# Performance work log

Hardware: AMD Instinct MI355X
Metric: run time of the kernel (lower is better)

Reference implementation:

```python
import jax, jax.numpy as jnp
import numpy as np

N, E, D = 50000, 800000, 128  # nodes, edges, in_dim == out_dim


def setup_inputs() -> dict:
    key = jax.random.key(0)
    ks = jax.random.split(key, 10)
    s = 1.0 / np.sqrt(2 * D)
    t = 1.0 / np.sqrt(D)
    return {
        "x": jax.random.normal(ks[0], (N, D), dtype=jnp.float32),
        "edge_index": jax.random.randint(ks[1], (2, E), 0, N, dtype=jnp.int64),
        # message_net: Linear(2D -> D), ReLU, Linear(D -> D)
        "mW1": jax.random.uniform(ks[2], (2 * D, D), jnp.float32, -s, s),
        "mb1": jax.random.uniform(ks[3], (D,), jnp.float32, -s, s),
        "mW2": jax.random.uniform(ks[4], (D, D), jnp.float32, -t, t),
        "mb2": jax.random.uniform(ks[5], (D,), jnp.float32, -t, t),
        # update_net: Linear(D + D -> D), ReLU, Linear(D -> D)
        "uW1": jax.random.uniform(ks[6], (2 * D, D), jnp.float32, -s, s),
        "ub1": jax.random.uniform(ks[7], (D,), jnp.float32, -s, s),
        "uW2": jax.random.uniform(ks[8], (D, D), jnp.float32, -t, t),
        "ub2": jax.random.uniform(ks[9], (D,), jnp.float32, -t, t),
    }


def reference(x, edge_index, mW1, mb1, mW2, mb2, uW1, ub1, uW2, ub2):
    row, col = edge_index[0], edge_index[1]
    # gather endpoints -> [E, 2D]
    msg_in = jnp.concatenate([x[row], x[col]], axis=-1)
    h = jax.nn.relu(msg_in @ mW1 + mb1)
    messages = h @ mW2 + mb2  # [E, D]
    # scatter-add messages to destination nodes (index_add_ on col)
    aggregated = jax.ops.segment_sum(messages, col, num_segments=x.shape[0])
    upd_in = jnp.concatenate([x, aggregated], axis=-1)  # [N, 2D]
    g = jax.nn.relu(upd_in @ uW1 + ub1)
    return jax.nn.relu(g @ uW2 + ub2)
```

## Files before the change

kernel.cpp:

```cpp
#include <hip/hip_runtime.h>
#include <stdint.h>

typedef unsigned short ushort_t;

#define NNODES 50000
#define NEDGES 800000
#define DD 128
#define EB 128

typedef short bf16x8 __attribute__((ext_vector_type(8)));
typedef float f32x16 __attribute__((ext_vector_type(16)));

#define XH_OFF    0u
#define XL_OFF    12800000u
#define W1P_OFF   25600000u
#define W2P_OFF   25731072u
#define WS_MIN    25796608u
#define DEG_OFF   25796608u
#define ELIST_OFF 25996800u
#define CUR_OFF   29196800u
#define WS_CSR    29396992u

#define PQ_OFF2   0u
#define W1P_OFF2  51200000u
#define U2P_OFF2  51331072u
#define WNP_OFF2  51396608u
#define W2U_OFF2  51527680u
#define VV_OFF2   51593216u
#define DEG_OFF2  51593728u
#define CUR_OFF2  51793920u
#define BSUM_OFF2 51994112u
#define EL_OFF2   51994368u
#define WS_NEW    55194368u
#define WS_NEW2   58394368u

#define NB_SCAN 49

__global__ void zero_kernel(float4* __restrict__ p, int n4) {
    int i = blockIdx.x * blockDim.x + threadIdx.x;
    if (i < n4) p[i] = make_float4(0.f, 0.f, 0.f, 0.f);
}
__global__ void zero_i32(int* __restrict__ p, int n) {
    int i = blockIdx.x * blockDim.x + threadIdx.x;
    if (i < n) p[i] = 0;
}

__device__ inline void bf16_split(float f, ushort_t& hi, ushort_t& lo) {
    uint32_t b = __float_as_uint(f);
    uint32_t hb = b & 0xFFFF0000u;
    hi = (ushort_t)(b >> 16);
    float lof = f - __uint_as_float(hb);
    lo = (ushort_t)(__float_as_uint(lof) >> 16);
}

__global__ void pack_x(const float* __restrict__ x,
                       ushort_t* __restrict__ xh, ushort_t* __restrict__ xl) {
    int i = blockIdx.x * blockDim.x + threadIdx.x;
    if (i >= NNODES * DD) return;
    ushort_t h, l;
    bf16_split(x[i], h, l);
    xh[i] = h; xl[i] = l;
}

__global__ void pack_w(const float* __restrict__ W, ushort_t* __restrict__ wp,
                       int K) {
    int i = blockIdx.x * blockDim.x + threadIdx.x;
    if (i >= K * 128) return;
    int k = i >> 7, n = i & 127;
    int base = (k >> 4) * 4096 + ((((k >> 3) & 1) * 128 + n) << 3) + (k & 7);
    ushort_t h, l;
    bf16_split(W[i], h, l);
    wp[base] = h; wp[base + 2048] = l;
}

__global__ void pack3(const float* __restrict__ mW1, const float* __restrict__ uW2,
                      const float* __restrict__ uW1,
                      ushort_t* __restrict__ w1p, ushort_t* __restrict__ u2p,
                      ushort_t* __restrict__ wnp) {
    int i = blockIdx.x * blockDim.x + threadIdx.x;
    const float* W; ushort_t* wp; int li;
    if (i < 32768)      { W = mW1; wp = w1p; li = i; }
    else if (i < 49152) { W = uW2; wp = u2p; li = i - 32768; }
    else                { W = uW1; wp = wnp; li = i - 49152; }
    int k = li >> 7, n = li & 127;
    int base = (k >> 4) * 4096 + ((((k >> 3) & 1) * 128 + n) << 3) + (k & 7);
    ushort_t h, l;
    bf16_split(W[li], h, l);
    wp[base] = h; wp[base + 2048] = l;
}

__global__ void hist_kernel(const int* __restrict__ ei, int* __restrict__ deg) {
    int i = blockIdx.x * blockDim.x + threadIdx.x;
    if (i < NEDGES) atomicAdd(&deg[ei[NEDGES + i]], 1);
}

__global__ __launch_bounds__(1024)
void scan_kernel(const int* __restrict__ deg, int* __restrict__ cursor) {
    __shared__ int part[1024];
    const int t = threadIdx.x;
    const int CH = 49;
    int s = 0;
#pragma unroll 1
    for (int i = 0; i < CH; ++i) {
        int idx = t * CH + i;
        if (idx < NNODES) s += deg[idx];
    }
    part[t] = s;
    __syncthreads();
    for (int d = 1; d < 1024; d <<= 1) {
        int v = (t >= d) ? part[t - d] : 0;
        __syncthreads();
        part[t] += v;
        __syncthreads();
    }
    int run = (t == 0) ? 0 : part[t - 1];
#pragma unroll 1
    for (int i = 0; i < CH; ++i) {
        int idx = t * CH + i;
        if (idx < NNODES) {
            cursor[idx] = run;
            run += deg[idx];
        }
    }
}

__global__ __launch_bounds__(1024)
void scanA(const int* __restrict__ deg, int* __restrict__ cur,
           int* __restrict__ bsum) {
    __shared__ int sm[1024];
    const int t = threadIdx.x;
    const int idx = blockIdx.x * 1024 + t;
    int d = (idx < NNODES) ? deg[idx] : 0;
    sm[t] = d;
    __syncthreads();
    for (int off = 1; off < 1024; off <<= 1) {
        int v = 0;
        if (t >= off) v = sm[t - off];
        __syncthreads();
        sm[t] += v;
        __syncthreads();
    }
    if (idx < NNODES) cur[idx] = sm[t];
    if (t == 1023) bsum[blockIdx.x] = sm[1023];
}
__global__ void scanB(int* __restrict__ bsum, int nb) {
    if (threadIdx.x == 0) {
        int run = 0;
        for (int i = 0; i < nb; ++i) { int v = bsum[i]; bsum[i] = run; run += v; }
    }
}
__global__ __launch_bounds__(1024)
void scanC(const int* __restrict__ deg, int* __restrict__ cur,
           const int* __restrict__ bsum) {
    const int idx = blockIdx.x * 1024 + threadIdx.x;
    if (idx < NNODES) cur[idx] = cur[idx] - deg[idx] + bsum[blockIdx.x];
}
__global__ __launch_bounds__(1024)
void scanC2(const int* __restrict__ deg, int* __restrict__ cur,
            const int* __restrict__ bsum) {
    int pre = 0;
#pragma unroll 1
    for (int j = 0; j < blockIdx.x; ++j) pre += bsum[j];
    const int idx = blockIdx.x * 1024 + threadIdx.x;
    if (idx < NNODES) cur[idx] = cur[idx] - deg[idx] + pre;
}

__global__ void fill_kernel(const int* __restrict__ ei, int* __restrict__ cursor,
                            int* __restrict__ elist) {
    int i = blockIdx.x * blockDim.x + threadIdx.x;
    if (i < NEDGES) {
        int pos = atomicAdd(&cursor[ei[NEDGES + i]], 1);
        elist[pos] = i;
    }
}
__global__ void fill2_kernel(const int* __restrict__ ei, int* __restrict__ cursor,
                             int2* __restrict__ ep) {
    int i = blockIdx.x * blockDim.x + threadIdx.x;
    if (i < NEDGES) {
        int c = ei[NEDGES + i];
        int pos = atomicAdd(&cursor[c], 1);
        ep[pos] = make_int2(ei[i], c);
    }
}

__global__ void w2u_kernel(const float* __restrict__ W2,
                           const float* __restrict__ U1, float* __restrict__ W2U) {
    int id = blockIdx.x * 256 + threadIdx.x;
    if (id >= 128 * 128) return;
    int i = id >> 7, j = id & 127;
    float s = 0.f;
    for (int k = 0; k < 128; ++k) s += W2[i * 128 + k] * U1[(128 + k) * 128 + j];
    W2U[id] = s;
}
__global__ void vvec_kernel(const float* __restrict__ b2,
                            const float* __restrict__ U1, float* __restrict__ vv) {
    int j = threadIdx.x;
    if (j >= 128) return;
    float s = 0.f;
    for (int k = 0; k < 128; ++k) s += b2[k] * U1[(128 + k) * 128 + j];
    vv[j] = s;
}
__global__ void w2u_vv(const float* __restrict__ W2, const float* __restrict__ b2,
                       const float* __restrict__ U1,
                       float* __restrict__ W2U, float* __restrict__ vv) {
    if (blockIdx.x < 64) {
        int id = blockIdx.x * 256 + threadIdx.x;
        int i = id >> 7, j = id & 127;
        float s = 0.f;
        for (int k = 0; k < 128; ++k)
            s += W2[i * 128 + k] * U1[(128 + k) * 128 + j];
        W2U[id] = s;
    } else if (threadIdx.x < 128) {
        int j = threadIdx.x;
        float s = 0.f;
        for (int k = 0; k < 128; ++k)
            s += b2[k] * U1[(128 + k) * 128 + j];
        vv[j] = s;
    }
}

__global__ __launch_bounds__(256)
void pq_gemm(const float* __restrict__ x, const ushort_t* __restrict__ w1p,
             const float* __restrict__ b1, float* __restrict__ PQ) {
    __shared__ __align__(16) ushort_t Wst[4096];
    const int t = threadIdx.x, w = t >> 6, l = t & 63;
    const int lh = l >> 5, ln = l & 31;
    const int base = blockIdx.x * 128;
    const int c = blockIdx.y;
    const int row = base + w * 32 + ln;
    const float* ax = x + (size_t)min(row, NNODES - 1) * DD;
    const ushort_t* wt = w1p + c * 8 * 4096;

    f32x16 acc[4];
#pragma unroll
    for (int tt = 0; tt < 4; ++tt)
#pragma unroll
        for (int q = 0; q < 16; ++q) acc[tt][q] = 0.f;

    float4 pfh = *(const float4*)(wt + t * 8);
    float4 pfl = *(const float4*)(wt + 2048 + t * 8);
    for (int u = 0; u < 8; ++u) {
        __syncthreads();
        *(float4*)(Wst + t * 8)        = pfh;
        *(float4*)(Wst + 2048 + t * 8) = pfl;
        float4 a0 = *(const float4*)(ax + u * 16 + lh * 8);
        float4 a1 = *(const float4*)(ax + u * 16 + lh * 8 + 4);
        if (u < 7) {
            pfh = *(const float4*)(wt + (u + 1) * 4096 + t * 8);
            pfl = *(const float4*)(wt + (u + 1) * 4096 + 2048 + t * 8);
        }
        float av[8] = {a0.x, a0.y, a0.z, a0.w, a1.x, a1.y, a1.z, a1.w};
        bf16x8 a_hi, a_lo;
#pragma unroll
        for (int q = 0; q < 8; ++q) {
            ushort_t h, lo16;
            bf16_split(av[q], h, lo16);
            a_hi[q] = (short)h; a_lo[q] = (short)lo16;
        }
        __syncthreads();
#pragma unroll
        for (int tt = 0; tt < 4; ++tt) {
            const int boff = (lh * 128 + tt * 32 + ln) * 8;
            bf16x8 bh = *(const bf16x8*)(Wst + boff);
            bf16x8 bl = *(const bf16x8*)(Wst + 2048 + boff);
            acc[tt] = __builtin_amdgcn_mfma_f32_32x32x16_bf16(a_hi, bh, acc[tt], 0, 0, 0);
            acc[tt] = __builtin_amdgcn_mfma_f32_32x32x16_bf16(a_hi, bl, acc[tt], 0, 0, 0);
            acc[tt] = __builtin_amdgcn_mfma_f32_32x32x16_bf16(a_lo, bh, acc[tt], 0, 0, 0);
        }
    }
    float bias[4];
#pragma unroll
    for (int tt = 0; tt < 4; ++tt)
        bias[tt] = (c == 0) ? b1[tt * 32 + ln] : 0.f;
#pragma unroll
    for (int tt = 0; tt < 4; ++tt) {
#pragma unroll
        for (int r = 0; r < 16; ++r) {
            int mrow = w * 32 + (r & 3) + 8 * (r >> 2) + 4 * lh;
            int n = base + mrow;
            if (n < NNODES)
                PQ[(size_t)n * 256 + c * 128 + tt * 32 + ln] = acc[tt][r] + bias[tt];
        }
    }
}

#define EW_C 4
__global__ __launch_bounds__(256)
void edge_ew(const float* __restrict__ PQ, const int* __restrict__ ei,
             const int* __restrict__ elist, float* Hsum) {
    const int t = threadIdx.x, w = t >> 6, l = t & 63;
    const int start = blockIdx.x * 512 + w * 128;
    if (start >= NEDGES) return;
    const int end = min(start + 128, NEDGES);

    float sx = 0.f, sy = 0.f;
    int cur = -1;
    int rv[EW_C] = {0, 0, 0, 0}, cv[EW_C] = {0, 0, 0, 0};
    float px[EW_C] = {0, 0, 0, 0}, py[EW_C] = {0, 0, 0, 0};
    float qx[EW_C] = {0, 0, 0, 0}, qy[EW_C] = {0, 0, 0, 0};

    const int navail = min(EW_C, end - start);
#pragma unroll
    for (int i = 0; i < EW_C; ++i)
        if (i < navail) {
            int e = elist[start + i];
            rv[i] = ei[e]; cv[i] = ei[NEDGES + e];
        }
#pragma unroll
    for (int i = 0; i < EW_C; ++i)
        if (i < navail) {
            float2 p = *(const float2*)(PQ + (size_t)rv[i] * 256 + 2 * l);
            float2 q = *(const float2*)(PQ + (size_t)cv[i] * 256 + 128 + 2 * l);
            px[i] = p.x; py[i] = p.y; qx[i] = q.x; qy[i] = q.y;
        }

    for (int pos = start; pos < end; pos += EW_C) {
        const int cnt = min(EW_C, end - pos);
        int nn = end - (pos + EW_C);
        nn = nn < 0 ? 0 : (nn > EW_C ? EW_C : nn);
        int nrv[EW_C] = {0, 0, 0, 0}, ncv[EW_C] = {0, 0, 0, 0};
        float npx[EW_C] = {0, 0, 0, 0}, npy[EW_C] = {0, 0, 0, 0};
        float nqx[EW_C] = {0, 0, 0, 0}, nqy[EW_C] = {0, 0, 0, 0};
#pragma unroll
        for (int i = 0; i < EW_C; ++i)
            if (i < nn) {
                int e = elist[pos + EW_C + i];
                nrv[i] = ei[e]; ncv[i] = ei[NEDGES + e];
            }
#pragma unroll
        for (int i = 0; i < EW_C; ++i)
            if (i < nn) {
                float2 p = *(const float2*)(PQ + (size_t)nrv[i] * 256 + 2 * l);
                float2 q = *(const float2*)(PQ + (size_t)ncv[i] * 256 + 128 + 2 * l);
                npx[i] = p.x; npy[i] = p.y; nqx[i] = q.x; nqy[i] = q.y;
            }
#pragma unroll
        for (int i = 0; i < EW_C; ++i)
            if (i < cnt) {
                if (cv[i] != cur) {
                    if (cur >= 0) {
                        atomicAdd(Hsum + (size_t)cur * DD + 2 * l,     sx);
                        atomicAdd(Hsum + (size_t)cur * DD + 2 * l + 1, sy);
                    }
                    sx = 0.f; sy = 0.f; cur = cv[i];
                }
                sx += fmaxf(px[i] + qx[i], 0.f);
                sy += fmaxf(py[i] + qy[i], 0.f);
            }
#pragma unroll
        for (int i = 0; i < EW_C; ++i) {
            rv[i] = nrv[i]; cv[i] = ncv[i];
            px[i] = npx[i]; py[i] = npy[i]; qx[i] = nqx[i]; qy[i] = nqy[i];
        }
    }
    if (cur >= 0) {
        atomicAdd(Hsum + (size_t)cur * DD + 2 * l,     sx);
        atomicAdd(Hsum + (size_t)cur * DD + 2 * l + 1, sy);
    }
}

__global__ __launch_bounds__(256)
void edge_pn(const float* __restrict__ PQ, const int2* __restrict__ ep,
             const int* __restrict__ endp, const int* __restrict__ deg,
             float* __restrict__ Hsum) {
    const int n = blockIdx.x * 4 + (threadIdx.x >> 6);
    if (n >= NNODES) return;
    const int l = threadIdx.x & 63;
    const int end = endp[n];
    const int start = end - deg[n];

    const float2 q = *(const float2*)(PQ + (size_t)n * 256 + 128 + 2 * l);
    float sx = 0.f, sy = 0.f;

    int s0[4];
    float2 p0[4];
    const int c0 = min(4, end - start);
#pragma unroll
    for (int i = 0; i < 4; ++i) s0[i] = (i < c0) ? ep[start + i].x : 0;
#pragma unroll
    for (int i = 0; i < 4; ++i)
        if (i < c0) p0[i] = *(const float2*)(PQ + (size_t)s0[i] * 256 + 2 * l);

    for (int e = start; e < end; e += 4) {
        const int cnt = min(4, end - e);
        int nn = end - (e + 4);
        nn = nn < 0 ? 0 : (nn > 4 ? 4 : nn);
        int s1[4];
        float2 p1[4];
#pragma unroll
        for (int i = 0; i < 4; ++i) s1[i] = (i < nn) ? ep[e + 4 + i].x : 0;
#pragma unroll
        for (int i = 0; i < 4; ++i)
            if (i < nn) p1[i] = *(const float2*)(PQ + (size_t)s1[i] * 256 + 2 * l);
#pragma unroll
        for (int i = 0; i < 4; ++i)
            if (i < cnt) {
                sx += fmaxf(p0[i].x + q.x, 0.f);
                sy += fmaxf(p0[i].y + q.y, 0.f);
            }
#pragma unroll
        for (int i = 0; i < 4; ++i) { s0[i] = s1[i]; p0[i] = p1[i]; }
    }

    Hsum[(size_t)n * DD + 2 * l]     = sx;
    Hsum[(size_t)n * DD + 2 * l + 1] = sy;
}

__device__ inline int hs_idx(int m, int j) {
    return m * 128 + ((((j >> 2) ^ (m & 31)) << 2) | (j & 3));
}

__global__ __launch_bounds__(256, 2)
void node_mfma(const float* __restrict__ x, float* outHsum,
               const ushort_t* __restrict__ wnp, const ushort_t* __restrict__ u2p,
               const int* __restrict__ deg, const float* __restrict__ vv,
               const float* __restrict__ ub1, const float* __restrict__ ub2) {
    __shared__ __align__(16) float    Hs[128 * 128];
    __shared__ __align__(16) ushort_t Wst[4096];
    const int t = threadIdx.x, w = t >> 6, l = t & 63;
    const int lh = l >> 5, ln = l & 31;
    const int base = blockIdx.x * 128;
    const int row = base + w * 32 + ln;
    const int rowc = min(row, NNODES - 1);
    const float* ax = x + (size_t)rowc * DD;
    const float* ah = outHsum + (size_t)rowc * DD;

    f32x16 acc[4];
#pragma unroll
    for (int tt = 0; tt < 4; ++tt)
#pragma unroll
        for (int q = 0; q < 16; ++q) acc[tt][q] = 0.f;

    float4 pfh = *(const float4*)(wnp + t * 8);
    float4 pfl = *(const float4*)(wnp + 2048 + t * 8);
    for (int u = 0; u < 16; ++u) {
        __syncthreads();
        *(float4*)(Wst + t * 8)        = pfh;
        *(float4*)(Wst + 2048 + t * 8) = pfl;
        const int k = u * 16 + lh * 8;
        const float* src = (k < 128) ? (ax + k) : (ah + (k - 128));
        float4 a0 = *(const float4*)(src);
        float4 a1 = *(const float4*)(src + 4);
        if (u < 15) {
            pfh = *(const float4*)(wnp + (u + 1) * 4096 + t * 8);
            pfl = *(const float4*)(wnp + (u + 1) * 4096 + 2048 + t * 8);
        }
        float av[8] = {a0.x, a0.y, a0.z, a0.w, a1.x, a1.y, a1.z, a1.w};
        bf16x8 a_hi, a_lo;
#pragma unroll
        for (int q = 0; q < 8; ++q) {
            ushort_t h, lo16;
            bf16_split(av[q], h, lo16);
            a_hi[q] = (short)h; a_lo[q] = (short)lo16;
        }
        __syncthreads();
#pragma unroll
        for (int tt = 0; tt < 4; ++tt) {
            const int boff = (lh * 128 + tt * 32 + ln) * 8;
            bf16x8 bh = *(const bf16x8*)(Wst + boff);
            bf16x8 bl = *(const bf16x8*)(Wst + 2048 + boff);
            acc[tt] = __builtin_amdgcn_mfma_f32_32x32x16_bf16(a_hi, bh, acc[tt], 0, 0, 0);
            acc[tt] = __builtin_amdgcn_mfma_f32_32x32x16_bf16(a_hi, bl, acc[tt], 0, 0, 0);
            acc[tt] = __builtin_amdgcn_mfma_f32_32x32x16_bf16(a_lo, bh, acc[tt], 0, 0, 0);
        }
    }

    float4 pfh2 = *(const float4*)(u2p + t * 8);
    float4 pfl2 = *(const float4*)(u2p + 2048 + t * 8);

    float b1v[4], vvv[4];
#pragma unroll
    for (int tt = 0; tt < 4; ++tt) {
        b1v[tt] = ub1[tt * 32 + ln];
        vvv[tt] = vv[tt * 32 + ln];
    }
#pragma unroll
    for (int tt = 0; tt < 4; ++tt) {
#pragma unroll
        for (int r = 0; r < 16; ++r) {
            int mrow = w * 32 + (r & 3) + 8 * (r >> 2) + 4 * lh;
            int n = min(base + mrow, NNODES - 1);
            float dg = (float)deg[n];
            float g = acc[tt][r] + b1v[tt] + dg * vvv[tt];
            Hs[hs_idx(mrow, tt * 32 + ln)] = fmaxf(g, 0.f);
            acc[tt][r] = 0.f;
        }
    }

    for (int u = 0; u < 8; ++u) {
        __syncthreads();
        *(float4*)(Wst + t * 8)        = pfh2;
        *(float4*)(Wst + 2048 + t * 8) = pfl2;
        if (u < 7) {
            pfh2 = *(const float4*)(u2p + (u + 1) * 4096 + t * 8);
            pfl2 = *(const float4*)(u2p + (u + 1) * 4096 + 2048 + t * 8);
        }
        __syncthreads();
        const int m  = w * 32 + ln;
        const int s0 = u * 4 + lh * 2;
        float4 f0 = *(const float4*)(Hs + m * 128 + (((s0    ) ^ ln) << 2));
        float4 f1 = *(const float4*)(Hs + m * 128 + (((s0 + 1) ^ ln) << 2));
        float fv[8] = {f0.x, f0.y, f0.z, f0.w, f1.x, f1.y, f1.z, f1.w};
        bf16x8 a_hi, a_lo;
#pragma unroll
        for (int q = 0; q < 8; ++q) {
            ushort_t h, lo16;
            bf16_split(fv[q], h, lo16);
            a_hi[q] = (short)h; a_lo[q] = (short)lo16;
        }
#pragma unroll
        for (int tt = 0; tt < 4; ++tt) {
            const int boff = (lh * 128 + tt * 32 + ln) * 8;
            bf16x8 bh = *(const bf16x8*)(Wst + boff);
            bf16x8 bl = *(const bf16x8*)(Wst + 2048 + boff);
            acc[tt] = __builtin_amdgcn_mfma_f32_32x32x16_bf16(a_hi, bh, acc[tt], 0, 0, 0);
            acc[tt] = __builtin_amdgcn_mfma_f32_32x32x16_bf16(a_hi, bl, acc[tt], 0, 0, 0);
            acc[tt] = __builtin_amdgcn_mfma_f32_32x32x16_bf16(a_lo, bh, acc[tt], 0, 0, 0);
        }
    }

    float b2v[4];
#pragma unroll
    for (int tt = 0; tt < 4; ++tt) b2v[tt] = ub2[tt * 32 + ln];
#pragma unroll
    for (int tt = 0; tt < 4; ++tt) {
#pragma unroll
        for (int r = 0; r < 16; ++r) {
            int mrow = w * 32 + (r & 3) + 8 * (r >> 2) + 4 * lh;
            int n = base + mrow;
            if (n < NNODES)
                outHsum[(size_t)n * DD + tt * 32 + ln] =
                    fmaxf(acc[tt][r] + b2v[tt], 0.f);
        }
    }
}

template <int MODE>
__global__ __launch_bounds__(256, 2)
void edge_mfma(const ushort_t* __restrict__ xh, const ushort_t* __restrict__ xl,
               const ushort_t* __restrict__ w1p, const ushort_t* __restrict__ w2p,
               const int* __restrict__ ei, const int* __restrict__ elist,
               const float* __restrict__ b1, const float* __restrict__ b2,
               float* agg) {
    __shared__ __align__(16) float    Hsl[128 * 128];
    __shared__ __align__(16) ushort_t Wst[4096];
    const int t  = threadIdx.x;
    const int w  = t >> 6;
    const int l  = t & 63;
    const int lh = l >> 5;
    const int ln = l & 31;
    int eg;
    if (MODE == 1) eg = elist[blockIdx.x * EB + w * 32 + ln];
    else           eg = blockIdx.x * EB + w * 32 + ln;
    const int rv = ei[eg];
    const int cv = ei[NEDGES + eg];
    float bias1[4], bias2[4];
#pragma unroll
    for (int tt = 0; tt < 4; ++tt) {
        bias1[tt] = b1[tt * 32 + ln];
        bias2[tt] = b2[tt * 32 + ln];
    }
    f32x16 acc[4];
#pragma unroll
    for (int tt = 0; tt < 4; ++tt)
#pragma unroll
        for (int q = 0; q < 16; ++q) acc[tt][q] = 0.f;
    bf16x8 a_hi_next = *(const bf16x8*)(xh + (size_t)rv * DD + lh * 8);
    bf16x8 a_lo_next = *(const bf16x8*)(xl + (size_t)rv * DD + lh * 8);
    float4 pfh = *(const float4*)(w1p + t * 8);
    float4 pfl = *(const float4*)(w1p + 2048 + t * 8);
    for (int u = 0; u < 16; ++u) {
        __syncthreads();
        *(float4*)(Wst + t * 8)        = pfh;
        *(float4*)(Wst + 2048 + t * 8) = pfl;
        bf16x8 a_hi = a_hi_next, a_lo = a_lo_next;
        if (u < 15) {
            pfh = *(const float4*)(w1p + (u + 1) * 4096 + t * 8);
            pfl = *(const float4*)(w1p + (u + 1) * 4096 + 2048 + t * 8);
            int kk = (u + 1) * 16 + lh * 8;
            const int node = (kk < 128) ? rv : cv;
            const int off  = kk & 127;
            a_hi_next = *(const bf16x8*)(xh + (size_t)node * DD + off);
            a_lo_next = *(const bf16x8*)(xl + (size_t)node * DD + off);
        }
        __syncthreads();
#pragma unroll
        for (int tt = 0; tt < 4; ++tt) {
            const int boff = (lh * 128 + tt * 32 + ln) * 8;
            bf16x8 bh = *(const bf16x8*)(Wst + boff);
            bf16x8 bl = *(const bf16x8*)(Wst + 2048 + boff);
            acc[tt] = __builtin_amdgcn_mfma_f32_32x32x16_bf16(a_hi, bh, acc[tt], 0, 0, 0);
            acc[tt] = __builtin_amdgcn_mfma_f32_32x32x16_bf16(a_hi, bl, acc[tt], 0, 0, 0);
            acc[tt] = __builtin_amdgcn_mfma_f32_32x32x16_bf16(a_lo, bh, acc[tt], 0, 0, 0);
        }
    }
    pfh = *(const float4*)(w2p + t * 8);
    pfl = *(const float4*)(w2p + 2048 + t * 8);
#pragma unroll
    for (int tt = 0; tt < 4; ++tt) {
#pragma unroll
        for (int r = 0; r < 16; ++r) {
            int mrow = w * 32 + (r & 3) + 8 * (r >> 2) + 4 * lh;
            int j    = tt * 32 + ln;
            Hsl[hs_idx(mrow, j)] = fmaxf(acc[tt][r] + bias1[tt], 0.f);
            acc[tt][r] = 0.f;
        }
    }
    for (int u = 0; u < 8; ++u) {
        __syncthreads();
        *(float4*)(Wst + t * 8)        = pfh;
        *(float4*)(Wst + 2048 + t * 8) = pfl;
        if (u < 7) {
            pfh = *(const float4*)(w2p + (u + 1) * 4096 + t * 8);
            pfl = *(const float4*)(w2p + (u + 1) * 4096 + 2048 + t * 8);
        }
        __syncthreads();
        const int m  = w * 32 + ln;
        const int s0 = u * 4 + lh * 2;
        float4 f0 = *(const float4*)(Hsl + m * 128 + (((s0    ) ^ ln) << 2));
        float4 f1 = *(const float4*)(Hsl + m * 128 + (((s0 + 1) ^ ln) << 2));
        float fv[8] = {f0.x, f0.y, f0.z, f0.w, f1.x, f1.y, f1.z, f1.w};
        bf16x8 a_hi, a_lo;
#pragma unroll
        for (int q = 0; q < 8; ++q) {
            ushort_t h, lo16;
            bf16_split(fv[q], h, lo16);
            a_hi[q] = (short)h;
            a_lo[q] = (short)lo16;
        }
#pragma unroll
        for (int tt = 0; tt < 4; ++tt) {
            const int boff = (lh * 128 + tt * 32 + ln) * 8;
            bf16x8 bh = *(const bf16x8*)(Wst + boff);
            bf16x8 bl = *(const bf16x8*)(Wst + 2048 + boff);
            acc[tt] = __builtin_amdgcn_mfma_f32_32x32x16_bf16(a_hi, bh, acc[tt], 0, 0, 0);
            acc[tt] = __builtin_amdgcn_mfma_f32_32x32x16_bf16(a_hi, bl, acc[tt], 0, 0, 0);
            acc[tt] = __builtin_amdgcn_mfma_f32_32x32x16_bf16(a_lo, bh, acc[tt], 0, 0, 0);
        }
    }
    if (MODE == 1) {
        float s[4] = {0.f, 0.f, 0.f, 0.f};
        int cur = __shfl(cv, 0, 64);
#pragma unroll
        for (int row = 0; row < 32; ++row) {
            const int r = (row & 3) | ((row >> 3) << 2);
            const int h = (row >> 2) & 1;
            int nd = __shfl(cv, row, 64);
            if (nd != cur) {
                if (lh == 0) {
#pragma unroll
                    for (int tt = 0; tt < 4; ++tt)
                        atomicAdd(agg + (size_t)cur * DD + tt * 32 + ln, s[tt]);
                }
#pragma unroll
                for (int tt = 0; tt < 4; ++tt) s[tt] = 0.f;
                cur = nd;
            }
#pragma unroll
            for (int tt = 0; tt < 4; ++tt) {
                float mine  = acc[tt][r];
                float other = __shfl_xor(mine, 32, 64);
                float v = (h == lh) ? mine : other;
                s[tt] += v + bias2[tt];
            }
        }
        if (lh == 0) {
#pragma unroll
            for (int tt = 0; tt < 4; ++tt)
                atomicAdd(agg + (size_t)cur * DD + tt * 32 + ln, s[tt]);
        }
    } else {
        int cn[16];
#pragma unroll
        for (int r = 0; r < 16; ++r) {
            int mr = (r & 3) + 8 * (r >> 2) + 4 * lh;
            cn[r] = __shfl(cv, mr, 64);
        }
#pragma unroll
        for (int tt = 0; tt < 4; ++tt) {
#pragma unroll
            for (int r = 0; r < 16; ++r) {
                atomicAdd(agg + (size_t)cn[r] * DD + tt * 32 + ln,
                          acc[tt][r] + bias2[tt]);
            }
        }
    }
}

#define TE 64
#define KT 16
#define AX_S 260
#define HS_S 132
#define AX_WORDS (TE * AX_S)
#define WT_WORDS (KT * DD)
#define SMEM_WORDS (AX_WORDS + WT_WORDS + TE)

__global__ __launch_bounds__(256, 2)
void node_kernel(const float* __restrict__ x,
                 float* aggout,
                 const float* __restrict__ U1, const float* __restrict__ c1,
                 const float* __restrict__ U2, const float* __restrict__ c2) {
    __shared__ float smem[SMEM_WORDS];
    float* Ax = smem;
    float* Hss = smem;
    float* Wt = smem + AX_WORDS;
    const int t = threadIdx.x;
    const int base = blockIdx.x * TE;
    {
        const int e = t & 63;
        const int q = t >> 6;
        const int n = base + e;
        const bool valid = n < NNODES;
        const float* s1 = x + (size_t)n * DD;
        const float* s2 = aggout + (size_t)n * DD;
#pragma unroll
        for (int ci = 0; ci < 16; ++ci) {
            const int k4 = ci * 4 + q;
            float4 v = make_float4(0.f, 0.f, 0.f, 0.f);
            if (valid) {
                if (k4 < 32) v = *(const float4*)(s1 + k4 * 4);
                else         v = *(const float4*)(s2 + (k4 - 32) * 4);
            }
            *(float4*)(Ax + e * AX_S + k4 * 4) = v;
        }
    }
    const int jg = t & 31;
    const int eg2 = t >> 5;
    const int j0 = jg * 4;
    const float4 b1v = *(const float4*)(c1 + j0);
    const float4 b2v = *(const float4*)(c2 + j0);
    float acc[8][4];
#pragma unroll
    for (int i = 0; i < 8; ++i)
        acc[i][0] = acc[i][1] = acc[i][2] = acc[i][3] = 0.f;
    for (int kb = 0; kb < 256 / KT; ++kb) {
        __syncthreads();
        {
            const float* src = U1 + kb * KT * DD;
#pragma unroll
            for (int u = 0; u < 2; ++u) {
                const int f4i = u * 256 + t;
                *(float4*)(Wt + f4i * 4) = *(const float4*)(src + f4i * 4);
            }
        }
        __syncthreads();
        float4 Bc[KT];
#pragma unroll
        for (int kk = 0; kk < KT; ++kk)
            Bc[kk] = *(const float4*)(Wt + kk * DD + j0);
#pragma unroll
        for (int i = 0; i < 8; ++i) {
            const float* arow = Ax + (i * 8 + eg2) * AX_S + kb * KT;
            float a[KT];
#pragma unroll
            for (int kc = 0; kc < KT / 4; ++kc) {
                const float4 av = *(const float4*)(arow + kc * 4);
                a[kc * 4 + 0] = av.x; a[kc * 4 + 1] = av.y;
                a[kc * 4 + 2] = av.z; a[kc * 4 + 3] = av.w;
            }
#pragma unroll
            for (int kk = 0; kk < KT; ++kk) {
                acc[i][0] = fmaf(a[kk], Bc[kk].x, acc[i][0]);
                acc[i][1] = fmaf(a[kk], Bc[kk].y, acc[i][1]);
                acc[i][2] = fmaf(a[kk], Bc[kk].z, acc[i][2]);
                acc[i][3] = fmaf(a[kk], Bc[kk].w, acc[i][3]);
            }
        }
    }
    __syncthreads();
#pragma unroll
    for (int i = 0; i < 8; ++i) {
        float4 h;
        h.x = fmaxf(acc[i][0] + b1v.x, 0.f);
        h.y = fmaxf(acc[i][1] + b1v.y, 0.f);
        h.z = fmaxf(acc[i][2] + b1v.z, 0.f);
        h.w = fmaxf(acc[i][3] + b1v.w, 0.f);
        *(float4*)(Hss + (i * 8 + eg2) * HS_S + j0) = h;
        acc[i][0] = acc[i][1] = acc[i][2] = acc[i][3] = 0.f;
    }
    for (int kb = 0; kb < DD / KT; ++kb) {
        __syncthreads();
        {
            const float* src = U2 + kb * KT * DD;
#pragma unroll
            for (int u = 0; u < 2; ++u) {
                const int f4i = u * 256 + t;
                *(float4*)(Wt + f4i * 4) = *(const float4*)(src + f4i * 4);
            }
        }
        __syncthreads();
        float4 Bc[KT];
#pragma unroll
        for (int kk = 0; kk < KT; ++kk)
            Bc[kk] = *(const float4*)(Wt + kk * DD + j0);
#pragma unroll
        for (int i = 0; i < 8; ++i) {
            const float* arow = Hss + (i * 8 + eg2) * HS_S + kb * KT;
            float a[KT];
#pragma unroll
            for (int kc = 0; kc < KT / 4; ++kc) {
                const float4 av = *(const float4*)(arow + kc * 4);
                a[kc * 4 + 0] = av.x; a[kc * 4 + 1] = av.y;
                a[kc * 4 + 2] = av.z; a[kc * 4 + 3] = av.w;
            }
#pragma unroll
            for (int kk = 0; kk < KT; ++kk) {
                acc[i][0] = fmaf(a[kk], Bc[kk].x, acc[i][0]);
                acc[i][1] = fmaf(a[kk], Bc[kk].y, acc[i][1]);
                acc[i][2] = fmaf(a[kk], Bc[kk].z, acc[i][2]);
                acc[i][3] = fmaf(a[kk], Bc[kk].w, acc[i][3]);
            }
        }
    }
#pragma unroll
    for (int i = 0; i < 8; ++i) {
        const int n = base + i * 8 + eg2;
        if (n < NNODES) {
            float4 o;
            o.x = fmaxf(acc[i][0] + b2v.x, 0.f);
            o.y = fmaxf(acc[i][1] + b2v.y, 0.f);
            o.z = fmaxf(acc[i][2] + b2v.z, 0.f);
            o.w = fmaxf(acc[i][3] + b2v.w, 0.f);
            *(float4*)(aggout + (size_t)n * DD + j0) = o;
        }
    }
}

extern "C" void kernel_launch(void* const* d_in, const int* in_sizes, int n_in,
                              void* d_out, int out_size, void* d_ws, size_t ws_size,
                              hipStream_t stream) {
    const float* x   = (const float*)d_in[0];
    const int*   ei  = (const int*)d_in[1];
    const float* mW1 = (const float*)d_in[2];
    const float* mb1 = (const float*)d_in[3];
    const float* mW2 = (const float*)d_in[4];
    const float* mb2 = (const float*)d_in[5];
    const float* uW1 = (const float*)d_in[6];
    const float* ub1 = (const float*)d_in[7];
    const float* uW2 = (const float*)d_in[8];
    const float* ub2 = (const float*)d_in[9];
    float* out = (float*)d_out;

    const int n4 = NNODES * DD / 4;

    if (ws_size >= (size_t)WS_NEW) {
        float*    PQ   = (float*)((char*)d_ws + PQ_OFF2);
        ushort_t* w1p  = (ushort_t*)((char*)d_ws + W1P_OFF2);
        ushort_t* u2p  = (ushort_t*)((char*)d_ws + U2P_OFF2);
        ushort_t* wnp  = (ushort_t*)((char*)d_ws + WNP_OFF2);
        float*    W2U  = (float*)((char*)d_ws + W2U_OFF2);
        float*    vv   = (float*)((char*)d_ws + VV_OFF2);
        int*      deg  = (int*)((char*)d_ws + DEG_OFF2);
        int*      curb = (int*)((char*)d_ws + CUR_OFF2);
        int*      bsum = (int*)((char*)d_ws + BSUM_OFF2);

        if (ws_size >= (size_t)WS_NEW2) {
            int2* ep = (int2*)((char*)d_ws + EL_OFF2);
            zero_i32<<<(50048 + 255) / 256, 256, 0, stream>>>(deg, 50048);
            hist_kernel<<<(NEDGES + 255) / 256, 256, 0, stream>>>(ei, deg);
            scanA<<<NB_SCAN, 1024, 0, stream>>>(deg, curb, bsum);
            scanC2<<<NB_SCAN, 1024, 0, stream>>>(deg, curb, bsum);
            fill2_kernel<<<(NEDGES + 255) / 256, 256, 0, stream>>>(ei, curb, ep);
            pack3<<<256, 256, 0, stream>>>(mW1, uW2, uW1, w1p, u2p, wnp);
            w2u_vv<<<65, 256, 0, stream>>>(mW2, mb2, uW1, W2U, vv);
            pack_w<<<(128 * 128 + 255) / 256, 256, 0, stream>>>(W2U, wnp + 32768, 128);
            pq_gemm<<<dim3(391, 2), 256, 0, stream>>>(x, w1p, mb1, PQ);
            edge_pn<<<(NNODES + 3) / 4, 256, 0, stream>>>(PQ, ep, curb, deg, out);
            node_mfma<<<391, 256, 0, stream>>>(x, out, wnp, u2p, deg, vv, ub1, ub2);
        } else {
            int* elst = (int*)((char*)d_ws + EL_OFF2);
            zero_kernel<<<(n4 + 255) / 256, 256, 0, stream>>>((float4*)out, n4);
            zero_i32<<<(50048 + 255) / 256, 256, 0, stream>>>(deg, 50048);
            hist_kernel<<<(NEDGES + 255) / 256, 256, 0, stream>>>(ei, deg);
            scanA<<<NB_SCAN, 1024, 0, stream>>>(deg, curb, bsum);
            scanB<<<1, 64, 0, stream>>>(bsum, NB_SCAN);
            scanC<<<NB_SCAN, 1024, 0, stream>>>(deg, curb, bsum);
            fill_kernel<<<(NEDGES + 255) / 256, 256, 0, stream>>>(ei, curb, elst);
            pack_w<<<(256 * 128 + 255) / 256, 256, 0, stream>>>(mW1, w1p, 256);
            pack_w<<<(128 * 128 + 255) / 256, 256, 0, stream>>>(uW2, u2p, 128);
            w2u_kernel<<<64, 256, 0, stream>>>(mW2, uW1, W2U);
            vvec_kernel<<<1, 128, 0, stream>>>(mb2, uW1, vv);
            pack_w<<<(128 * 128 + 255) / 256, 256, 0, stream>>>(uW1, wnp, 128);
            pack_w<<<(128 * 128 + 255) / 256, 256, 0, stream>>>(W2U, wnp + 32768, 128);
            pq_gemm<<<dim3(391, 2), 256, 0, stream>>>(x, w1p, mb1, PQ);
            edge_ew<<<(NEDGES + 511) / 512, 256, 0, stream>>>(PQ, ei, elst, out);
            node_mfma<<<391, 256, 0, stream>>>(x, out, wnp, u2p, deg, vv, ub1, ub2);
        }
        return;
    }

    zero_kernel<<<(n4 + 255) / 256, 256, 0, stream>>>((float4*)out, n4);
    if (ws_size >= (size_t)WS_MIN) {
        ushort_t* xh  = (ushort_t*)((char*)d_ws + XH_OFF);
        ushort_t* xl  = (ushort_t*)((char*)d_ws + XL_OFF);
        ushort_t* w1p = (ushort_t*)((char*)d_ws + W1P_OFF);
        ushort_t* w2p = (ushort_t*)((char*)d_ws + W2P_OFF);
        pack_x<<<(NNODES * DD + 255) / 256, 256, 0, stream>>>(x, xh, xl);
        pack_w<<<(256 * 128 + 255) / 256, 256, 0, stream>>>(mW1, w1p, 256);
        pack_w<<<(128 * 128 + 255) / 256, 256, 0, stream>>>(mW2, w2p, 128);
        if (ws_size >= (size_t)WS_CSR) {
            int* deg    = (int*)((char*)d_ws + DEG_OFF);
            int* elist  = (int*)((char*)d_ws + ELIST_OFF);
            int* cursor = (int*)((char*)d_ws + CUR_OFF);
            zero_i32<<<(50048 + 255) / 256, 256, 0, stream>>>(deg, 50048);
            hist_kernel<<<(NEDGES + 255) / 256, 256, 0, stream>>>(ei, deg);
            scan_kernel<<<1, 1024, 0, stream>>>(deg, cursor);
            fill_kernel<<<(NEDGES + 255) / 256, 256, 0, stream>>>(ei, cursor, elist);
            edge_mfma<1><<<NEDGES / EB, 256, 0, stream>>>(
                xh, xl, w1p, w2p, ei, elist, mb1, mb2, out);
        } else {
            edge_mfma<0><<<NEDGES / EB, 256, 0, stream>>>(
                xh, xl, w1p, w2p, ei, (const int*)nullptr, mb1, mb2, out);
        }
    }
    node_kernel<<<(NNODES + TE - 1) / TE, 256, 0, stream>>>(x, out, uW1, ub1,
                                                            uW2, ub2);
}
```

Before: 322.0 us.

## Merge prep kernels, shrink CSR edge list, retile node MLP to 64-row blocks

```diff
diff --git a/kernel.cpp b/kernel.cpp
--- a/kernel.cpp
+++ b/kernel.cpp
@@ -73,20 +73,25 @@
     wp[base] = h; wp[base + 2048] = l;
 }
 
-__global__ void pack3(const float* __restrict__ mW1, const float* __restrict__ uW2,
+__global__ void prep0(const float* __restrict__ mW1, const float* __restrict__ uW2,
                       const float* __restrict__ uW1,
                       ushort_t* __restrict__ w1p, ushort_t* __restrict__ u2p,
-                      ushort_t* __restrict__ wnp) {
-    int i = blockIdx.x * blockDim.x + threadIdx.x;
-    const float* W; ushort_t* wp; int li;
-    if (i < 32768)      { W = mW1; wp = w1p; li = i; }
-    else if (i < 49152) { W = uW2; wp = u2p; li = i - 32768; }
-    else                { W = uW1; wp = wnp; li = i - 49152; }
-    int k = li >> 7, n = li & 127;
-    int base = (k >> 4) * 4096 + ((((k >> 3) & 1) * 128 + n) << 3) + (k & 7);
-    ushort_t h, l;
-    bf16_split(W[li], h, l);
-    wp[base] = h; wp[base + 2048] = l;
+                      ushort_t* __restrict__ wnp, int* __restrict__ deg) {
+    if (blockIdx.x < 256) {
+        int i = blockIdx.x * 256 + threadIdx.x;
+        const float* W; ushort_t* wp; int li;
+        if (i < 32768)      { W = mW1; wp = w1p; li = i; }
+        else if (i < 49152) { W = uW2; wp = u2p; li = i - 32768; }
+        else                { W = uW1; wp = wnp; li = i - 49152; }
+        int k = li >> 7, n = li & 127;
+        int base = (k >> 4) * 4096 + ((((k >> 3) & 1) * 128 + n) << 3) + (k & 7);
+        ushort_t h, l;
+        bf16_split(W[li], h, l);
+        wp[base] = h; wp[base + 2048] = l;
+    } else {
+        int j = (blockIdx.x - 256) * 256 + threadIdx.x;
+        if (j < 50048) deg[j] = 0;
+    }
 }
 
 __global__ void hist_kernel(const int* __restrict__ ei, int* __restrict__ deg) {
@@ -173,13 +178,12 @@
         elist[pos] = i;
     }
 }
-__global__ void fill2_kernel(const int* __restrict__ ei, int* __restrict__ cursor,
-                             int2* __restrict__ ep) {
+__global__ void fill3_kernel(const int* __restrict__ ei, int* __restrict__ cursor,
+                             int* __restrict__ srcs) {
     int i = blockIdx.x * blockDim.x + threadIdx.x;
     if (i < NEDGES) {
-        int c = ei[NEDGES + i];
-        int pos = atomicAdd(&cursor[c], 1);
-        ep[pos] = make_int2(ei[i], c);
+        int pos = atomicAdd(&cursor[ei[NEDGES + i]], 1);
+        srcs[pos] = ei[i];
     }
 }
 
@@ -200,16 +204,19 @@
     for (int k = 0; k < 128; ++k) s += b2[k] * U1[(128 + k) * 128 + j];
     vv[j] = s;
 }
-__global__ void w2u_vv(const float* __restrict__ W2, const float* __restrict__ b2,
-                       const float* __restrict__ U1,
-                       float* __restrict__ W2U, float* __restrict__ vv) {
+__global__ void w2u_vv_pack(const float* __restrict__ W2, const float* __restrict__ b2,
+                            const float* __restrict__ U1,
+                            ushort_t* __restrict__ wnp2, float* __restrict__ vv) {
     if (blockIdx.x < 64) {
         int id = blockIdx.x * 256 + threadIdx.x;
         int i = id >> 7, j = id & 127;
         float s = 0.f;
         for (int k = 0; k < 128; ++k)
             s += W2[i * 128 + k] * U1[(128 + k) * 128 + j];
-        W2U[id] = s;
+        int base = (i >> 4) * 4096 + ((((i >> 3) & 1) * 128 + j) << 3) + (i & 7);
+        ushort_t h, l;
+        bf16_split(s, h, l);
+        wnp2[base] = h; wnp2[base + 2048] = l;
     } else if (threadIdx.x < 128) {
         int j = threadIdx.x;
         float s = 0.f;
@@ -360,9 +367,9 @@
 }
 
 __global__ __launch_bounds__(256)
-void edge_pn(const float* __restrict__ PQ, const int2* __restrict__ ep,
-             const int* __restrict__ endp, const int* __restrict__ deg,
-             float* __restrict__ Hsum) {
+void edge_pn2(const float* __restrict__ PQ, const int* __restrict__ srcs,
+              const int* __restrict__ endp, const int* __restrict__ deg,
+              float* __restrict__ Hsum) {
     const int n = blockIdx.x * 4 + (threadIdx.x >> 6);
     if (n >= NNODES) return;
     const int l = threadIdx.x & 63;
@@ -376,7 +383,7 @@
     float2 p0[4];
     const int c0 = min(4, end - start);
 #pragma unroll
-    for (int i = 0; i < 4; ++i) s0[i] = (i < c0) ? ep[start + i].x : 0;
+    for (int i = 0; i < 4; ++i) s0[i] = (i < c0) ? srcs[start + i] : 0;
 #pragma unroll
     for (int i = 0; i < 4; ++i)
         if (i < c0) p0[i] = *(const float2*)(PQ + (size_t)s0[i] * 256 + 2 * l);
@@ -388,7 +395,7 @@
         int s1[4];
         float2 p1[4];
 #pragma unroll
-        for (int i = 0; i < 4; ++i) s1[i] = (i < nn) ? ep[e + 4 + i].x : 0;
+        for (int i = 0; i < 4; ++i) s1[i] = (i < nn) ? srcs[e + 4 + i] : 0;
 #pragma unroll
         for (int i = 0; i < 4; ++i)
             if (i < nn) p1[i] = *(const float2*)(PQ + (size_t)s1[i] * 256 + 2 * l);
@@ -408,6 +415,145 @@
 
 __device__ inline int hs_idx(int m, int j) {
     return m * 128 + ((((j >> 2) ^ (m & 31)) << 2) | (j & 3));
+}
+
+__global__ __launch_bounds__(128)
+void node_mfma2(const float* __restrict__ x, float* outHsum,
+                const ushort_t* __restrict__ wnp, const ushort_t* __restrict__ u2p,
+                const int* __restrict__ deg, const float* __restrict__ vv,
+                const float* __restrict__ ub1, const float* __restrict__ ub2) {
+    __shared__ __align__(16) float    Hs[64 * 128];
+    __shared__ __align__(16) ushort_t Wst[4096];
+    const int t = threadIdx.x, w = t >> 6, l = t & 63;
+    const int lh = l >> 5, ln = l & 31;
+    const int base = blockIdx.x * 64;
+    const int row = base + w * 32 + ln;
+    const int rowc = min(row, NNODES - 1);
+    const float* ax = x + (size_t)rowc * DD;
+    const float* ah = outHsum + (size_t)rowc * DD;
+
+    f32x16 acc[4];
+#pragma unroll
+    for (int tt = 0; tt < 4; ++tt)
+#pragma unroll
+        for (int q = 0; q < 16; ++q) acc[tt][q] = 0.f;
+
+    float4 pfh0 = *(const float4*)(wnp + t * 8);
+    float4 pfh1 = *(const float4*)(wnp + (t + 128) * 8);
+    float4 pfl0 = *(const float4*)(wnp + 2048 + t * 8);
+    float4 pfl1 = *(const float4*)(wnp + 2048 + (t + 128) * 8);
+    for (int u = 0; u < 16; ++u) {
+        __syncthreads();
+        *(float4*)(Wst + t * 8)                = pfh0;
+        *(float4*)(Wst + (t + 128) * 8)        = pfh1;
+        *(float4*)(Wst + 2048 + t * 8)         = pfl0;
+        *(float4*)(Wst + 2048 + (t + 128) * 8) = pfl1;
+        const int k = u * 16 + lh * 8;
+        const float* src = (k < 128) ? (ax + k) : (ah + (k - 128));
+        float4 a0 = *(const float4*)(src);
+        float4 a1 = *(const float4*)(src + 4);
+        if (u < 15) {
+            const ushort_t* nx = wnp + (u + 1) * 4096;
+            pfh0 = *(const float4*)(nx + t * 8);
+            pfh1 = *(const float4*)(nx + (t + 128) * 8);
+            pfl0 = *(const float4*)(nx + 2048 + t * 8);
+            pfl1 = *(const float4*)(nx + 2048 + (t + 128) * 8);
+        }
+        float av[8] = {a0.x, a0.y, a0.z, a0.w, a1.x, a1.y, a1.z, a1.w};
+        bf16x8 a_hi, a_lo;
+#pragma unroll
+        for (int q = 0; q < 8; ++q) {
+            ushort_t h, lo16;
+            bf16_split(av[q], h, lo16);
+            a_hi[q] = (short)h; a_lo[q] = (short)lo16;
+        }
+        __syncthreads();
+#pragma unroll
+        for (int tt = 0; tt < 4; ++tt) {
+            const int boff = (lh * 128 + tt * 32 + ln) * 8;
+            bf16x8 bh = *(const bf16x8*)(Wst + boff);
+            bf16x8 bl = *(const bf16x8*)(Wst + 2048 + boff);
+            acc[tt] = __builtin_amdgcn_mfma_f32_32x32x16_bf16(a_hi, bh, acc[tt], 0, 0, 0);
+            acc[tt] = __builtin_amdgcn_mfma_f32_32x32x16_bf16(a_hi, bl, acc[tt], 0, 0, 0);
+            acc[tt] = __builtin_amdgcn_mfma_f32_32x32x16_bf16(a_lo, bh, acc[tt], 0, 0, 0);
+        }
+    }
+
+    float4 p2h0 = *(const float4*)(u2p + t * 8);
+    float4 p2h1 = *(const float4*)(u2p + (t + 128) * 8);
+    float4 p2l0 = *(const float4*)(u2p + 2048 + t * 8);
+    float4 p2l1 = *(const float4*)(u2p + 2048 + (t + 128) * 8);
+
+    float b1v[4], vvv[4];
+#pragma unroll
+    for (int tt = 0; tt < 4; ++tt) {
+        b1v[tt] = ub1[tt * 32 + ln];
+        vvv[tt] = vv[tt * 32 + ln];
+    }
+#pragma unroll
+    for (int tt = 0; tt < 4; ++tt) {
+#pragma unroll
+        for (int r = 0; r < 16; ++r) {
+            int mrow = w * 32 + (r & 3) + 8 * (r >> 2) + 4 * lh;
+            int n = min(base + mrow, NNODES - 1);
+            float dg = (float)deg[n];
+            float g = acc[tt][r] + b1v[tt] + dg * vvv[tt];
+            Hs[hs_idx(mrow, tt * 32 + ln)] = fmaxf(g, 0.f);
+            acc[tt][r] = 0.f;
+        }
+    }
+
+    for (int u = 0; u < 8; ++u) {
+        __syncthreads();
+        *(float4*)(Wst + t * 8)                = p2h0;
+        *(float4*)(Wst + (t + 128) * 8)        = p2h1;
+        *(float4*)(Wst + 2048 + t * 8)         = p2l0;
+        *(float4*)(Wst + 2048 + (t + 128) * 8) = p2l1;
+        if (u < 7) {
+            const ushort_t* nx = u2p + (u + 1) * 4096;
+            p2h0 = *(const float4*)(nx + t * 8);
+            p2h1 = *(const float4*)(nx + (t + 128) * 8);
+            p2l0 = *(const float4*)(nx + 2048 + t * 8);
+            p2l1 = *(const float4*)(nx + 2048 + (t + 128) * 8);
+        }
+        __syncthreads();
+        const int m  = w * 32 + ln;
+        const int s0 = u * 4 + lh * 2;
+        float4 f0 = *(const float4*)(Hs + m * 128 + (((s0    ) ^ ln) << 2));
+        float4 f1 = *(const float4*)(Hs + m * 128 + (((s0 + 1) ^ ln) << 2));
+        float fv[8] = {f0.x, f0.y, f0.z, f0.w, f1.x, f1.y, f1.z, f1.w};
+        bf16x8 a_hi, a_lo;
+#pragma unroll
+        for (int q = 0; q < 8; ++q) {
+            ushort_t h, lo16;
+            bf16_split(fv[q], h, lo16);
+            a_hi[q] = (short)h; a_lo[q] = (short)lo16;
+        }
+#pragma unroll
+        for (int tt = 0; tt < 4; ++tt) {
+            const int boff = (lh * 128 + tt * 32 + ln) * 8;
+            bf16x8 bh = *(const bf16x8*)(Wst + boff);
+            bf16x8 bl = *(const bf16x8*)(Wst + 2048 + boff);
+            acc[tt] = __builtin_amdgcn_mfma_f32_32x32x16_bf16(a_hi, bh, acc[tt], 0, 0, 0);
+            acc[tt] = __builtin_amdgcn_mfma_f32_32x32x16_bf16(a_hi, bl, acc[tt], 0, 0, 0);
+            acc[tt] = __builtin_amdgcn_mfma_f32_32x32x16_bf16(a_lo, bh, acc[tt], 0, 0, 0);
+        }
+    }
+
+    float b2v[4];
+#pragma unroll
+    for (int tt = 0; tt < 4; ++tt) b2v[tt] = ub2[tt * 32 + ln];
+#pragma unroll
+    for (int tt = 0; tt < 4; ++tt) {
+#pragma unroll
+        for (int r = 0; r < 16; ++r) {
+            int mrow = w * 32 + (r & 3) + 8 * (r >> 2) + 4 * lh;
+            int n = base + mrow;
+            if (n < NNODES)
+                outHsum[(size_t)n * DD + tt * 32 + ln] =
+                    fmaxf(acc[tt][r] + b2v[tt], 0.f);
+        }
+    }
 }
 
 __global__ __launch_bounds__(256, 2)
@@ -415,7 +561,7 @@
                const ushort_t* __restrict__ wnp, const ushort_t* __restrict__ u2p,
                const int* __restrict__ deg, const float* __restrict__ vv,
                const float* __restrict__ ub1, const float* __restrict__ ub2) {
-    __shared__ __align__(16) float    Hs[128 * 128];
+    __shared__ __align__(16) float    Hs2[128 * 128];
     __shared__ __align__(16) ushort_t Wst[4096];
     const int t = threadIdx.x, w = t >> 6, l = t & 63;
     const int lh = l >> 5, ln = l & 31;
@@ -482,7 +628,7 @@
             int n = min(base + mrow, NNODES - 1);
             float dg = (float)deg[n];
             float g = acc[tt][r] + b1v[tt] + dg * vvv[tt];
-            Hs[hs_idx(mrow, tt * 32 + ln)] = fmaxf(g, 0.f);
+            Hs2[hs_idx(mrow, tt * 32 + ln)] = fmaxf(g, 0.f);
             acc[tt][r] = 0.f;
         }
     }
@@ -498,8 +644,8 @@
         __syncthreads();
         const int m  = w * 32 + ln;
         const int s0 = u * 4 + lh * 2;
-        float4 f0 = *(const float4*)(Hs + m * 128 + (((s0    ) ^ ln) << 2));
-        float4 f1 = *(const float4*)(Hs + m * 128 + (((s0 + 1) ^ ln) << 2));
+        float4 f0 = *(const float4*)(Hs2 + m * 128 + (((s0    ) ^ ln) << 2));
+        float4 f1 = *(const float4*)(Hs2 + m * 128 + (((s0 + 1) ^ ln) << 2));
         float fv[8] = {f0.x, f0.y, f0.z, f0.w, f1.x, f1.y, f1.z, f1.w};
         bf16x8 a_hi, a_lo;
 #pragma unroll
@@ -855,18 +1001,17 @@
         int*      bsum = (int*)((char*)d_ws + BSUM_OFF2);
 
         if (ws_size >= (size_t)WS_NEW2) {
-            int2* ep = (int2*)((char*)d_ws + EL_OFF2);
-            zero_i32<<<(50048 + 255) / 256, 256, 0, stream>>>(deg, 50048);
+            int* srcs = (int*)((char*)d_ws + EL_OFF2);
+            prep0<<<452, 256, 0, stream>>>(mW1, uW2, uW1, w1p, u2p, wnp, deg);
             hist_kernel<<<(NEDGES + 255) / 256, 256, 0, stream>>>(ei, deg);
             scanA<<<NB_SCAN, 1024, 0, stream>>>(deg, curb, bsum);
             scanC2<<<NB_SCAN, 1024, 0, stream>>>(deg, curb, bsum);
-            fill2_kernel<<<(NEDGES + 255) / 256, 256, 0, stream>>>(ei, curb, ep);
-            pack3<<<256, 256, 0, stream>>>(mW1, uW2, uW1, w1p, u2p, wnp);
-            w2u_vv<<<65, 256, 0, stream>>>(mW2, mb2, uW1, W2U, vv);
-            pack_w<<<(128 * 128 + 255) / 256, 256, 0, stream>>>(W2U, wnp + 32768, 128);
+            fill3_kernel<<<(NEDGES + 255) / 256, 256, 0, stream>>>(ei, curb, srcs);
+            w2u_vv_pack<<<65, 256, 0, stream>>>(mW2, mb2, uW1, wnp + 32768, vv);
             pq_gemm<<<dim3(391, 2), 256, 0, stream>>>(x, w1p, mb1, PQ);
-            edge_pn<<<(NNODES + 3) / 4, 256, 0, stream>>>(PQ, ep, curb, deg, out);
-            node_mfma<<<391, 256, 0, stream>>>(x, out, wnp, u2p, deg, vv, ub1, ub2);
+            edge_pn2<<<(NNODES + 3) / 4, 256, 0, stream>>>(PQ, srcs, curb, deg, out);
+            node_mfma2<<<(NNODES + 63) / 64, 128, 0, stream>>>(
+                x, out, wnp, u2p, deg, vv, ub1, ub2);
         } else {
             int* elst = (int*)((char*)d_ws + EL_OFF2);
             zero_kernel<<<(n4 + 255) / 256, 256, 0, stream>>>((float4*)out, n4);
```

Result: faster. 315.0 us (-2.2%).
